# Kernel tuning notes

Hardware: AMD Instinct MI355X
Metric: run time of the kernel (lower is better)

Reference implementation:

```python
import jax, jax.numpy as jnp
import numpy as np

CHEB_K = 2  # Chebyshev polynomial order (init arg cheb_k)


def _avwgcn(x, E, w_pool, b_pool):
    """Adaptive Vertex-Wise Graph Convolution (AGCRN's AVWGCN).
    x: [B, N, C_in], E: [N, D], w_pool: [D, K, C_in, C_out], b_pool: [D, C_out].
    """
    N = E.shape[0]
    # adaptive adjacency from node embeddings
    supports = jax.nn.softmax(jax.nn.relu(E @ E.T), axis=1)  # [N, N]
    support_set = [jnp.eye(N, dtype=x.dtype), supports]
    for _ in range(2, CHEB_K):
        support_set.append(2.0 * supports @ support_set[-1] - support_set[-2])
    supports_k = jnp.stack(support_set)  # [K, N, N]
    # per-node adaptive weights/bias generated from embeddings
    weights = jnp.einsum('nd,dkio->nkio', E, w_pool)  # [N, K, C_in, C_out]
    bias = E @ b_pool  # [N, C_out]
    # graph propagation then per-node adaptive projection
    x_g = jnp.einsum('knm,bmc->bnkc', supports_k, x)  # [B, N, K, C_in]
    return jnp.einsum('bnki,nkio->bno', x_g, weights) + bias  # [B, N, C_out]


def setup_inputs() -> dict:
    key = jax.random.key(0)
    ks = jax.random.split(key, 7)
    B, N, DIN, DOUT, D = 64, 2048, 2, 64, 10
    return {
        'x': jax.random.normal(ks[0], (B, N, DIN), dtype=jnp.float32),
        'state': jax.random.normal(ks[1], (B, N, DOUT), dtype=jnp.float32),
        'node_embeddings': jax.random.normal(ks[2], (N, D), dtype=jnp.float32),
        'gate_w_pool': jax.random.normal(ks[3], (D, CHEB_K, DIN + DOUT, 2 * DOUT), dtype=jnp.float32) * 0.1,
        'gate_b_pool': jax.random.normal(ks[4], (D, 2 * DOUT), dtype=jnp.float32) * 0.1,
        'update_w_pool': jax.random.normal(ks[5], (D, CHEB_K, DIN + DOUT, DOUT), dtype=jnp.float32) * 0.1,
        'update_b_pool': jax.random.normal(ks[6], (D, DOUT), dtype=jnp.float32) * 0.1,
    }


def reference(x, state, node_embeddings, gate_w_pool, gate_b_pool, update_w_pool, update_b_pool):
    hidden_dim = state.shape[-1]
    input_and_state = jnp.concatenate([x, state], axis=-1)  # [B, N, DIN+DOUT]
    z_r = jax.nn.sigmoid(_avwgcn(input_and_state, node_embeddings, gate_w_pool, gate_b_pool))
    z, r = z_r[..., :hidden_dim], z_r[..., hidden_dim:]
    candidate = jnp.concatenate([x, z * state], axis=-1)
    hc = jnp.tanh(_avwgcn(candidate, node_embeddings, update_w_pool, update_b_pool))
    h = r * state + (1.0 - r) * hc
    return h
```

## Files before the change

kernel.cpp:

```cpp
#include <hip/hip_runtime.h>
#include <math.h>

#define N_NODES 2048
#define BATCH   64
#define DIN     2
#define DOUT    64
#define CIN     66
#define CP      68
#define D_EMB   10
#define GOUT    128
#define NCOLS   (BATCH*CP)
#define MK      2048
#define KTOT    132
#define LP      68

typedef __attribute__((ext_vector_type(8))) short bf16x8;
typedef __attribute__((ext_vector_type(8))) unsigned short u16x8;
typedef __attribute__((ext_vector_type(4))) float f32x4;

__device__ __forceinline__ unsigned short f2bf_rn(float f) {
    unsigned u = __builtin_bit_cast(unsigned, f);
    unsigned r = u + 0x7FFFu + ((u >> 16) & 1u);
    return (unsigned short)(r >> 16);
}
__device__ __forceinline__ float bf2f(unsigned short h) {
    unsigned u = ((unsigned)h) << 16;
    return __builtin_bit_cast(float, u);
}

__device__ __forceinline__ void gload_lds16(const void* g, void* l) {
    __builtin_amdgcn_global_load_lds(
        (const __attribute__((address_space(1))) unsigned int*)g,
        (__attribute__((address_space(3))) unsigned int*)l, 16, 0, 0);
}

__global__ __launch_bounds__(256) void supports_kernel(
    const float* __restrict__ E, unsigned short* __restrict__ S_hi)
{
    const int n   = blockIdx.x;
    const int tid = threadIdx.x;

    float en[D_EMB];
#pragma unroll
    for (int d = 0; d < D_EMB; ++d) en[d] = E[n * D_EMB + d];

    float vals[8];
    float mx = -1e30f;
#pragma unroll
    for (int j = 0; j < 8; ++j) {
        const int m = tid + j * 256;
        float dot = 0.f;
#pragma unroll
        for (int d = 0; d < D_EMB; ++d) dot += en[d] * E[m * D_EMB + d];
        dot = fmaxf(dot, 0.f);
        vals[j] = dot;
        mx = fmaxf(mx, dot);
    }

    __shared__ float sred[4];
    for (int off = 32; off > 0; off >>= 1) mx = fmaxf(mx, __shfl_xor(mx, off));
    if ((tid & 63) == 0) sred[tid >> 6] = mx;
    __syncthreads();
    mx = fmaxf(fmaxf(sred[0], sred[1]), fmaxf(sred[2], sred[3]));

    float sum = 0.f;
#pragma unroll
    for (int j = 0; j < 8; ++j) { vals[j] = __expf(vals[j] - mx); sum += vals[j]; }

    __syncthreads();
    for (int off = 32; off > 0; off >>= 1) sum += __shfl_xor(sum, off);
    if ((tid & 63) == 0) sred[tid >> 6] = sum;
    __syncthreads();
    sum = sred[0] + sred[1] + sred[2] + sred[3];

    const float inv = 1.f / sum;
#pragma unroll
    for (int j = 0; j < 8; ++j)
        S_hi[(size_t)n * N_NODES + tid + j * 256] = f2bf_rn(vals[j] * inv);
}

__global__ __launch_bounds__(256) void build_xt_kernel(
    const float* __restrict__ x, const float* __restrict__ state,
    const unsigned short* __restrict__ zs, const int use_zs,
    unsigned short* __restrict__ XT)
{
    const int b   = blockIdx.y;
    const int m0  = blockIdx.x * 64;
    const int tid = threadIdx.x;
    __shared__ float T[64][69];

    {
        const int r = tid >> 2;
        const int q = (tid & 3) * 16;
        if (use_zs) {
            const u16x8 v0 = *(const u16x8*)&zs[((size_t)(m0 + r) * BATCH + b) * DOUT + q];
            const u16x8 v1 = *(const u16x8*)&zs[((size_t)(m0 + r) * BATCH + b) * DOUT + q + 8];
#pragma unroll
            for (int u = 0; u < 8; ++u) {
                T[r][DIN + q + u]     = bf2f(v0[u]);
                T[r][DIN + q + 8 + u] = bf2f(v1[u]);
            }
        } else {
#pragma unroll
            for (int u = 0; u < 4; ++u) {
                const float4 v = *(const float4*)&state[((size_t)b * N_NODES + m0 + r) * DOUT + q + u * 4];
                T[r][DIN + q + u * 4 + 0] = v.x;
                T[r][DIN + q + u * 4 + 1] = v.y;
                T[r][DIN + q + u * 4 + 2] = v.z;
                T[r][DIN + q + u * 4 + 3] = v.w;
            }
        }
    }
    if (tid < 128) {
        const int r = tid >> 1, c = tid & 1;
        T[r][c] = x[((size_t)b * N_NODES + m0 + r) * DIN + c];
        T[r][CIN + c] = 0.f;
    }
    __syncthreads();

    for (int idx = tid; idx < CP * 64; idx += 256) {
        const int c  = idx >> 6;
        const int mm = idx & 63;
        XT[((size_t)(b * CP + c)) * N_NODES + m0 + mm] = f2bf_rn(T[mm][c]);
    }
}

__global__ __launch_bounds__(256) void gemm_mfma_kernel(
    const unsigned short* __restrict__ A,
    const unsigned short* __restrict__ BT, float* __restrict__ C)
{
    __shared__ __align__(16) unsigned short As[4096];
    __shared__ __align__(16) unsigned short Bs[4096];

    const int tid  = threadIdx.x;
    const int lane = tid & 63;
    const int w    = tid >> 6;
    const int wr   = w >> 1, wc = w & 1;
    const int bn   = blockIdx.x;
    const int bm   = blockIdx.y;

    f32x4 acc[4][4];
#pragma unroll
    for (int i = 0; i < 4; ++i)
#pragma unroll
        for (int j = 0; j < 4; ++j) acc[i][j] = (f32x4){0.f, 0.f, 0.f, 0.f};

    const int srow = ((tid >> 6) << 4) + (tid & 15);
    const int scol = ((tid >> 4) & 3) * 8;
    const unsigned a_off0 = (unsigned)(bm * 128 + srow) * MK + scol;
    const unsigned a_off1 = a_off0 + 64u * MK;
    const unsigned b_off0 = (unsigned)(bn * 128 + srow) * MK + scol;
    const unsigned b_off1 = b_off0 + 64u * MK;

    unsigned short* asl0 = As + tid * 8;
    unsigned short* asl1 = As + 2048 + tid * 8;
    unsigned short* bsl0 = Bs + tid * 8;
    unsigned short* bsl1 = Bs + 2048 + tid * 8;

#pragma unroll 1
    for (int k0 = 0; k0 < MK; k0 += 32) {
        gload_lds16(A  + a_off0 + k0, asl0);
        gload_lds16(A  + a_off1 + k0, asl1);
        gload_lds16(BT + b_off0 + k0, bsl0);
        gload_lds16(BT + b_off1 + k0, bsl1);
        __syncthreads();

        bf16x8 af[4], bf[4];
#pragma unroll
        for (int i = 0; i < 4; ++i)
            af[i] = *(const bf16x8*)(As + ((wr * 4 + i) * 64 + lane) * 8);
#pragma unroll
        for (int j = 0; j < 4; ++j)
            bf[j] = *(const bf16x8*)(Bs + ((wc * 4 + j) * 64 + lane) * 8);
#pragma unroll
        for (int i = 0; i < 4; ++i)
#pragma unroll
            for (int j = 0; j < 4; ++j)
                acc[i][j] = __builtin_amdgcn_mfma_f32_16x16x32_bf16(
                    af[i], bf[j], acc[i][j], 0, 0, 0);
        __syncthreads();
    }

    const int crow0 = bm * 128 + wr * 64;
    const int ccol0 = bn * 128 + wc * 64;
#pragma unroll
    for (int i = 0; i < 4; ++i)
#pragma unroll
        for (int j = 0; j < 4; ++j)
#pragma unroll
            for (int r = 0; r < 4; ++r) {
                const int row = crow0 + i * 16 + (lane >> 4) * 4 + r;
                const int col = ccol0 + j * 16 + (lane & 15);
                C[(size_t)row * NCOLS + col] = acc[i][j][r];
            }
}

__global__ __launch_bounds__(256) void gate_transform_kernel(
    const float* __restrict__ E, const float* __restrict__ wp,
    const float* __restrict__ bp, const float* __restrict__ x,
    const float* __restrict__ state, const float* __restrict__ AG,
    unsigned short* __restrict__ ZS, float* __restrict__ Rbuf)
{
    const int n     = blockIdx.x;
    const int ohalf = blockIdx.y;
    const int tid   = threadIdx.x;

    __shared__ float Wl[KTOT * LP];
    __shared__ float Il[KTOT * LP];
    __shared__ float bias_l[64];

    float en[D_EMB];
#pragma unroll
    for (int d = 0; d < D_EMB; ++d) en[d] = E[n * D_EMB + d];

    for (int idx = tid; idx < KTOT * 16; idx += 256) {
        const int kp = idx >> 4;
        const int o4 = (idx & 15) << 2;
        const float* wpp = wp + (size_t)kp * GOUT + ohalf * 64 + o4;
        float s0 = 0.f, s1 = 0.f, s2 = 0.f, s3 = 0.f;
#pragma unroll
        for (int d = 0; d < D_EMB; ++d) {
            const float4 v = *(const float4*)(wpp + (size_t)d * KTOT * GOUT);
            s0 += en[d] * v.x; s1 += en[d] * v.y;
            s2 += en[d] * v.z; s3 += en[d] * v.w;
        }
        *(float4*)&Wl[kp * LP + o4] = make_float4(s0, s1, s2, s3);
    }
    if (tid < 64) {
        float s = 0.f;
#pragma unroll
        for (int d = 0; d < D_EMB; ++d) s += en[d] * bp[d * GOUT + ohalf * 64 + tid];
        bias_l[tid] = s;
    }
    for (int idx = tid; idx < KTOT * BATCH; idx += 256) {
        const int kp = idx % KTOT;
        const int b  = idx / KTOT;
        float v;
        if (kp >= CIN)      v = AG[(size_t)n * NCOLS + b * CP + (kp - CIN)];
        else if (kp >= DIN) v = state[((size_t)b * N_NODES + n) * DOUT + kp - DIN];
        else                v = x[((size_t)b * N_NODES + n) * DIN + kp];
        Il[kp * LP + b] = v;
    }
    __syncthreads();

    const int og = (tid & 15) << 2;
    const int bg = (tid >> 4) << 2;

    float acc[4][4];
#pragma unroll
    for (int i = 0; i < 4; ++i)
#pragma unroll
        for (int j = 0; j < 4; ++j) acc[i][j] = 0.f;

    const float* Wb = Wl + og;
    const float* Ib = Il + bg;
#pragma unroll 4
    for (int kp = 0; kp < KTOT; ++kp) {
        const float4 wv = *(const float4*)(Wb + kp * LP);
        const float4 iv = *(const float4*)(Ib + kp * LP);
        const float wa[4] = {wv.x, wv.y, wv.z, wv.w};
        const float ia[4] = {iv.x, iv.y, iv.z, iv.w};
#pragma unroll
        for (int bi = 0; bi < 4; ++bi)
#pragma unroll
            for (int oi = 0; oi < 4; ++oi) acc[bi][oi] += ia[bi] * wa[oi];
    }

    if (ohalf == 0) {
#pragma unroll
        for (int bi = 0; bi < 4; ++bi) {
            const int b = bg + bi;
            const float4 st4 = *(const float4*)&state[((size_t)b * N_NODES + n) * DOUT + og];
            const float z0 = 1.f / (1.f + __expf(-(acc[bi][0] + bias_l[og + 0])));
            const float z1 = 1.f / (1.f + __expf(-(acc[bi][1] + bias_l[og + 1])));
            const float z2 = 1.f / (1.f + __expf(-(acc[bi][2] + bias_l[og + 2])));
            const float z3 = 1.f / (1.f + __expf(-(acc[bi][3] + bias_l[og + 3])));
            ushort4 zz;
            zz.x = f2bf_rn(z0 * st4.x); zz.y = f2bf_rn(z1 * st4.y);
            zz.z = f2bf_rn(z2 * st4.z); zz.w = f2bf_rn(z3 * st4.w);
            *(ushort4*)&ZS[((size_t)n * BATCH + b) * DOUT + og] = zz;
        }
    } else {
#pragma unroll
        for (int bi = 0; bi < 4; ++bi) {
            const int b = bg + bi;
            float4 rr;
            rr.x = 1.f / (1.f + __expf(-(acc[bi][0] + bias_l[og + 0])));
            rr.y = 1.f / (1.f + __expf(-(acc[bi][1] + bias_l[og + 1])));
            rr.z = 1.f / (1.f + __expf(-(acc[bi][2] + bias_l[og + 2])));
            rr.w = 1.f / (1.f + __expf(-(acc[bi][3] + bias_l[og + 3])));
            *(float4*)&Rbuf[((size_t)n * BATCH + b) * DOUT + og] = rr;
        }
    }
}

__global__ __launch_bounds__(256) void update_final_kernel(
    const float* __restrict__ E, const float* __restrict__ wp,
    const float* __restrict__ bp, const float* __restrict__ x,
    const unsigned short* __restrict__ ZS, const float* __restrict__ AG,
    const float* __restrict__ state, const float* __restrict__ Rbuf,
    float* __restrict__ out)
{
    const int n   = blockIdx.x;
    const int tid = threadIdx.x;

    __shared__ float Wl[KTOT * LP];
    __shared__ float Il[KTOT * LP];
    __shared__ float bias_l[64];

    float en[D_EMB];
#pragma unroll
    for (int d = 0; d < D_EMB; ++d) en[d] = E[n * D_EMB + d];

    for (int idx = tid; idx < KTOT * 16; idx += 256) {
        const int kp = idx >> 4;
        const int o4 = (idx & 15) << 2;
        const float* wpp = wp + (size_t)kp * DOUT + o4;
        float s0 = 0.f, s1 = 0.f, s2 = 0.f, s3 = 0.f;
#pragma unroll
        for (int d = 0; d < D_EMB; ++d) {
            const float4 v = *(const float4*)(wpp + (size_t)d * KTOT * DOUT);
            s0 += en[d] * v.x; s1 += en[d] * v.y;
            s2 += en[d] * v.z; s3 += en[d] * v.w;
        }
        *(float4*)&Wl[kp * LP + o4] = make_float4(s0, s1, s2, s3);
    }
    if (tid < 64) {
        float s = 0.f;
#pragma unroll
        for (int d = 0; d < D_EMB; ++d) s += en[d] * bp[d * DOUT + tid];
        bias_l[tid] = s;
    }
    for (int idx = tid; idx < KTOT * BATCH; idx += 256) {
        const int kp = idx % KTOT;
        const int b  = idx / KTOT;
        float v;
        if (kp >= CIN)      v = AG[(size_t)n * NCOLS + b * CP + (kp - CIN)];
        else if (kp >= DIN) v = bf2f(ZS[((size_t)n * BATCH + b) * DOUT + kp - DIN]);
        else                v = x[((size_t)b * N_NODES + n) * DIN + kp];
        Il[kp * LP + b] = v;
    }
    __syncthreads();

    const int og = (tid & 15) << 2;
    const int bg = (tid >> 4) << 2;

    float acc[4][4];
#pragma unroll
    for (int i = 0; i < 4; ++i)
#pragma unroll
        for (int j = 0; j < 4; ++j) acc[i][j] = 0.f;

    const float* Wb = Wl + og;
    const float* Ib = Il + bg;
#pragma unroll 4
    for (int kp = 0; kp < KTOT; ++kp) {
        const float4 wv = *(const float4*)(Wb + kp * LP);
        const float4 iv = *(const float4*)(Ib + kp * LP);
        const float wa[4] = {wv.x, wv.y, wv.z, wv.w};
        const float ia[4] = {iv.x, iv.y, iv.z, iv.w};
#pragma unroll
        for (int bi = 0; bi < 4; ++bi)
#pragma unroll
            for (int oi = 0; oi < 4; ++oi) acc[bi][oi] += ia[bi] * wa[oi];
    }

#pragma unroll
    for (int bi = 0; bi < 4; ++bi) {
        const int b = bg + bi;
        const float4 r4  = *(const float4*)&Rbuf[((size_t)n * BATCH + b) * DOUT + og];
        const float4 st4 = *(const float4*)&state[((size_t)b * N_NODES + n) * DOUT + og];
        float4 h;
        h.x = r4.x * st4.x + (1.f - r4.x) * tanhf(acc[bi][0] + bias_l[og + 0]);
        h.y = r4.y * st4.y + (1.f - r4.y) * tanhf(acc[bi][1] + bias_l[og + 1]);
        h.z = r4.z * st4.z + (1.f - r4.z) * tanhf(acc[bi][2] + bias_l[og + 2]);
        h.w = r4.w * st4.w + (1.f - r4.w) * tanhf(acc[bi][3] + bias_l[og + 3]);
        *(float4*)&out[((size_t)b * N_NODES + n) * DOUT + og] = h;
    }
}

extern "C" void kernel_launch(void* const* d_in, const int* in_sizes, int n_in,
                              void* d_out, int out_size, void* d_ws, size_t ws_size,
                              hipStream_t stream)
{
    const float* x  = (const float*)d_in[0];
    const float* st = (const float*)d_in[1];
    const float* E  = (const float*)d_in[2];
    const float* gw = (const float*)d_in[3];
    const float* gb = (const float*)d_in[4];
    const float* uw = (const float*)d_in[5];
    const float* ub = (const float*)d_in[6];
    float* out = (float*)d_out;

    unsigned short* S_hi = (unsigned short*)d_ws;
    unsigned short* XT   = S_hi + (size_t)N_NODES * N_NODES;
    float* AG = (float*)(XT + (size_t)NCOLS * N_NODES);
    unsigned short* ZS = (unsigned short*)(AG + (size_t)N_NODES * NCOLS);
    float* Rb = (float*)(ZS + (size_t)N_NODES * BATCH * DOUT);

    supports_kernel<<<N_NODES, 256, 0, stream>>>(E, S_hi);
    build_xt_kernel<<<dim3(N_NODES / 64, BATCH), 256, 0, stream>>>(x, st, ZS, 0, XT);
    gemm_mfma_kernel<<<dim3(NCOLS / 128, N_NODES / 128), 256, 0, stream>>>(S_hi, XT, AG);
    gate_transform_kernel<<<dim3(N_NODES, 2), 256, 0, stream>>>(E, gw, gb, x, st, AG, ZS, Rb);
    build_xt_kernel<<<dim3(N_NODES / 64, BATCH), 256, 0, stream>>>(x, st, ZS, 1, XT);
    gemm_mfma_kernel<<<dim3(NCOLS / 128, N_NODES / 128), 256, 0, stream>>>(S_hi, XT, AG);
    update_final_kernel<<<N_NODES, 256, 0, stream>>>(E, uw, ub, x, ZS, AG, st, Rb, out);
}
```

Before: 572.2 us.

## Move per-node gate/update projections to bf16 MFMA with split-weight precision

Replaces the scalar FP32 per-node projection loops in the gate and update kernels with 16x16x32 bf16 MFMA. Weights are split into hi/lo bf16 parts to keep accuracy, and inputs go into swizzled LDS fragments. A new pre-pass transposes the weight pools so per-node weight generation can use contiguous vector loads. The main GEMM grid is also remapped to a 1D launch with XCD-aware block ordering. The cost is two extra small launches, and the activations are now rounded to bf16, which may add error.

```diff
diff --git a/kernel.cpp b/kernel.cpp
--- a/kernel.cpp
+++ b/kernel.cpp
@@ -12,7 +12,7 @@
 #define NCOLS   (BATCH*CP)
 #define MK      2048
 #define KTOT    132
-#define LP      68
+#define KPAD    136
 
 typedef __attribute__((ext_vector_type(8))) short bf16x8;
 typedef __attribute__((ext_vector_type(8))) unsigned short u16x8;
@@ -32,6 +32,23 @@
     __builtin_amdgcn_global_load_lds(
         (const __attribute__((address_space(1))) unsigned int*)g,
         (__attribute__((address_space(3))) unsigned int*)l, 16, 0, 0);
+}
+
+__device__ __forceinline__ int frag_addr(int strip, int kt, int row, int slice) {
+    const int byte = ((strip * 5 + kt) * 16 + row) * 64 + slice * 16;
+    return byte ^ ((row & 7) << 4);
+}
+
+__global__ __launch_bounds__(256) void transpose_pool_kernel(
+    const float* __restrict__ wp, float* __restrict__ wpT, int OC, int total)
+{
+    const int idx = blockIdx.x * 256 + threadIdx.x;
+    if (idx >= total) return;
+    const int kp   = idx % KPAD;
+    const int rest = idx / KPAD;
+    const int o    = rest % OC;
+    const int d    = rest / OC;
+    wpT[idx] = (kp < KTOT) ? wp[((size_t)d * KTOT + kp) * OC + o] : 0.f;
 }
 
 __global__ __launch_bounds__(256) void supports_kernel(
@@ -136,8 +153,11 @@
     const int lane = tid & 63;
     const int w    = tid >> 6;
     const int wr   = w >> 1, wc = w & 1;
-    const int bn   = blockIdx.x;
-    const int bm   = blockIdx.y;
+
+    const int wg   = blockIdx.x;
+    const int wgid = (wg & 7) * 68 + (wg >> 3);
+    const int bn   = wgid % 34;
+    const int bm   = wgid / 34;
 
     f32x4 acc[4][4];
 #pragma unroll
@@ -195,8 +215,8 @@
             }
 }
 
-__global__ __launch_bounds__(256) void gate_transform_kernel(
-    const float* __restrict__ E, const float* __restrict__ wp,
+__global__ __launch_bounds__(256) void gate_mfma_kernel(
+    const float* __restrict__ E, const float* __restrict__ wpT,
     const float* __restrict__ bp, const float* __restrict__ x,
     const float* __restrict__ state, const float* __restrict__ AG,
     unsigned short* __restrict__ ZS, float* __restrict__ Rbuf)
@@ -205,26 +225,40 @@
     const int ohalf = blockIdx.y;
     const int tid   = threadIdx.x;
 
-    __shared__ float Wl[KTOT * LP];
-    __shared__ float Il[KTOT * LP];
+    __shared__ __align__(16) unsigned short INh[10240];
+    __shared__ __align__(16) unsigned short Whi[10240];
+    __shared__ __align__(16) unsigned short Wlo[10240];
     __shared__ float bias_l[64];
 
     float en[D_EMB];
 #pragma unroll
     for (int d = 0; d < D_EMB; ++d) en[d] = E[n * D_EMB + d];
 
-    for (int idx = tid; idx < KTOT * 16; idx += 256) {
-        const int kp = idx >> 4;
-        const int o4 = (idx & 15) << 2;
-        const float* wpp = wp + (size_t)kp * GOUT + ohalf * 64 + o4;
-        float s0 = 0.f, s1 = 0.f, s2 = 0.f, s3 = 0.f;
-#pragma unroll
-        for (int d = 0; d < D_EMB; ++d) {
-            const float4 v = *(const float4*)(wpp + (size_t)d * KTOT * GOUT);
-            s0 += en[d] * v.x; s1 += en[d] * v.y;
-            s2 += en[d] * v.z; s3 += en[d] * v.w;
-        }
-        *(float4*)&Wl[kp * LP + o4] = make_float4(s0, s1, s2, s3);
+    for (int slot = tid; slot < 1280; slot += 256) {
+        const int o = slot / 20, s = slot % 20;
+        float v[8] = {0.f, 0.f, 0.f, 0.f, 0.f, 0.f, 0.f, 0.f};
+        if (s < 17) {
+            const float* p = wpT + ((size_t)(ohalf * 64 + o)) * KPAD + s * 8;
+#pragma unroll
+            for (int d = 0; d < D_EMB; ++d) {
+                const float4 a = *(const float4*)(p + (size_t)d * GOUT * KPAD);
+                const float4 b = *(const float4*)(p + (size_t)d * GOUT * KPAD + 4);
+                v[0] += en[d] * a.x; v[1] += en[d] * a.y;
+                v[2] += en[d] * a.z; v[3] += en[d] * a.w;
+                v[4] += en[d] * b.x; v[5] += en[d] * b.y;
+                v[6] += en[d] * b.z; v[7] += en[d] * b.w;
+            }
+        }
+        u16x8 hv, lv;
+#pragma unroll
+        for (int u = 0; u < 8; ++u) {
+            const unsigned short h = f2bf_rn(v[u]);
+            hv[u] = h;
+            lv[u] = f2bf_rn(v[u] - bf2f(h));
+        }
+        const int addr = frag_addr(o >> 4, s >> 2, o & 15, s & 3);
+        *(u16x8*)((char*)Whi + addr) = hv;
+        *(u16x8*)((char*)Wlo + addr) = lv;
     }
     if (tid < 64) {
         float s = 0.f;
@@ -232,70 +266,69 @@
         for (int d = 0; d < D_EMB; ++d) s += en[d] * bp[d * GOUT + ohalf * 64 + tid];
         bias_l[tid] = s;
     }
-    for (int idx = tid; idx < KTOT * BATCH; idx += 256) {
-        const int kp = idx % KTOT;
-        const int b  = idx / KTOT;
-        float v;
-        if (kp >= CIN)      v = AG[(size_t)n * NCOLS + b * CP + (kp - CIN)];
-        else if (kp >= DIN) v = state[((size_t)b * N_NODES + n) * DOUT + kp - DIN];
-        else                v = x[((size_t)b * N_NODES + n) * DIN + kp];
-        Il[kp * LP + b] = v;
-    }
-    __syncthreads();
-
-    const int og = (tid & 15) << 2;
-    const int bg = (tid >> 4) << 2;
-
-    float acc[4][4];
-#pragma unroll
-    for (int i = 0; i < 4; ++i)
-#pragma unroll
-        for (int j = 0; j < 4; ++j) acc[i][j] = 0.f;
-
-    const float* Wb = Wl + og;
-    const float* Ib = Il + bg;
-#pragma unroll 4
-    for (int kp = 0; kp < KTOT; ++kp) {
-        const float4 wv = *(const float4*)(Wb + kp * LP);
-        const float4 iv = *(const float4*)(Ib + kp * LP);
-        const float wa[4] = {wv.x, wv.y, wv.z, wv.w};
-        const float ia[4] = {iv.x, iv.y, iv.z, iv.w};
-#pragma unroll
-        for (int bi = 0; bi < 4; ++bi)
-#pragma unroll
-            for (int oi = 0; oi < 4; ++oi) acc[bi][oi] += ia[bi] * wa[oi];
-    }
-
-    if (ohalf == 0) {
-#pragma unroll
-        for (int bi = 0; bi < 4; ++bi) {
-            const int b = bg + bi;
-            const float4 st4 = *(const float4*)&state[((size_t)b * N_NODES + n) * DOUT + og];
-            const float z0 = 1.f / (1.f + __expf(-(acc[bi][0] + bias_l[og + 0])));
-            const float z1 = 1.f / (1.f + __expf(-(acc[bi][1] + bias_l[og + 1])));
-            const float z2 = 1.f / (1.f + __expf(-(acc[bi][2] + bias_l[og + 2])));
-            const float z3 = 1.f / (1.f + __expf(-(acc[bi][3] + bias_l[og + 3])));
-            ushort4 zz;
-            zz.x = f2bf_rn(z0 * st4.x); zz.y = f2bf_rn(z1 * st4.y);
-            zz.z = f2bf_rn(z2 * st4.z); zz.w = f2bf_rn(z3 * st4.w);
-            *(ushort4*)&ZS[((size_t)n * BATCH + b) * DOUT + og] = zz;
-        }
-    } else {
-#pragma unroll
-        for (int bi = 0; bi < 4; ++bi) {
-            const int b = bg + bi;
-            float4 rr;
-            rr.x = 1.f / (1.f + __expf(-(acc[bi][0] + bias_l[og + 0])));
-            rr.y = 1.f / (1.f + __expf(-(acc[bi][1] + bias_l[og + 1])));
-            rr.z = 1.f / (1.f + __expf(-(acc[bi][2] + bias_l[og + 2])));
-            rr.w = 1.f / (1.f + __expf(-(acc[bi][3] + bias_l[og + 3])));
-            *(float4*)&Rbuf[((size_t)n * BATCH + b) * DOUT + og] = rr;
-        }
-    }
-}
-
-__global__ __launch_bounds__(256) void update_final_kernel(
-    const float* __restrict__ E, const float* __restrict__ wp,
+    for (int slot = tid; slot < 1280; slot += 256) {
+        const int b = slot / 20, s = slot % 20;
+        u16x8 hv;
+#pragma unroll
+        for (int u = 0; u < 8; ++u) {
+            const int k = s * 8 + u;
+            float v;
+            if (k < DIN)       v = x[((size_t)b * N_NODES + n) * DIN + k];
+            else if (k < CIN)  v = state[((size_t)b * N_NODES + n) * DOUT + k - DIN];
+            else if (k < KTOT) v = AG[(size_t)n * NCOLS + b * CP + (k - CIN)];
+            else               v = 0.f;
+            hv[u] = f2bf_rn(v);
+        }
+        *(u16x8*)((char*)INh + frag_addr(b >> 4, s >> 2, b & 15, s & 3)) = hv;
+    }
+    __syncthreads();
+
+    const int lane = tid & 63, w = tid >> 6;
+    const int row = lane & 15, sl = lane >> 4;
+
+    bf16x8 af[5];
+#pragma unroll
+    for (int kt = 0; kt < 5; ++kt)
+        af[kt] = *(const bf16x8*)((const char*)INh + frag_addr(w, kt, row, sl));
+
+    f32x4 acc[4];
+#pragma unroll
+    for (int j = 0; j < 4; ++j) acc[j] = (f32x4){0.f, 0.f, 0.f, 0.f};
+
+#pragma unroll
+    for (int j = 0; j < 4; ++j) {
+#pragma unroll
+        for (int kt = 0; kt < 5; ++kt) {
+            const bf16x8 bh = *(const bf16x8*)((const char*)Whi + frag_addr(j, kt, row, sl));
+            acc[j] = __builtin_amdgcn_mfma_f32_16x16x32_bf16(af[kt], bh, acc[j], 0, 0, 0);
+        }
+#pragma unroll
+        for (int kt = 0; kt < 5; ++kt) {
+            const bf16x8 bl = *(const bf16x8*)((const char*)Wlo + frag_addr(j, kt, row, sl));
+            acc[j] = __builtin_amdgcn_mfma_f32_16x16x32_bf16(af[kt], bl, acc[j], 0, 0, 0);
+        }
+    }
+
+#pragma unroll
+    for (int j = 0; j < 4; ++j) {
+        const int ol = j * 16 + row;
+        const float bs = bias_l[ol];
+#pragma unroll
+        for (int r = 0; r < 4; ++r) {
+            const int b = w * 16 + sl * 4 + r;
+            const float sg = 1.f / (1.f + __expf(-(acc[j][r] + bs)));
+            if (ohalf == 0) {
+                ZS[((size_t)n * BATCH + b) * DOUT + ol] =
+                    f2bf_rn(sg * state[((size_t)b * N_NODES + n) * DOUT + ol]);
+            } else {
+                Rbuf[((size_t)n * BATCH + b) * DOUT + ol] = sg;
+            }
+        }
+    }
+}
+
+__global__ __launch_bounds__(256) void update_mfma_kernel(
+    const float* __restrict__ E, const float* __restrict__ wpT,
     const float* __restrict__ bp, const float* __restrict__ x,
     const unsigned short* __restrict__ ZS, const float* __restrict__ AG,
     const float* __restrict__ state, const float* __restrict__ Rbuf,
@@ -304,26 +337,40 @@
     const int n   = blockIdx.x;
     const int tid = threadIdx.x;
 
-    __shared__ float Wl[KTOT * LP];
-    __shared__ float Il[KTOT * LP];
+    __shared__ __align__(16) unsigned short INh[10240];
+    __shared__ __align__(16) unsigned short Whi[10240];
+    __shared__ __align__(16) unsigned short Wlo[10240];
     __shared__ float bias_l[64];
 
     float en[D_EMB];
 #pragma unroll
     for (int d = 0; d < D_EMB; ++d) en[d] = E[n * D_EMB + d];
 
-    for (int idx = tid; idx < KTOT * 16; idx += 256) {
-        const int kp = idx >> 4;
-        const int o4 = (idx & 15) << 2;
-        const float* wpp = wp + (size_t)kp * DOUT + o4;
-        float s0 = 0.f, s1 = 0.f, s2 = 0.f, s3 = 0.f;
-#pragma unroll
-        for (int d = 0; d < D_EMB; ++d) {
-            const float4 v = *(const float4*)(wpp + (size_t)d * KTOT * DOUT);
-            s0 += en[d] * v.x; s1 += en[d] * v.y;
-            s2 += en[d] * v.z; s3 += en[d] * v.w;
-        }
-        *(float4*)&Wl[kp * LP + o4] = make_float4(s0, s1, s2, s3);
+    for (int slot = tid; slot < 1280; slot += 256) {
+        const int o = slot / 20, s = slot % 20;
+        float v[8] = {0.f, 0.f, 0.f, 0.f, 0.f, 0.f, 0.f, 0.f};
+        if (s < 17) {
+            const float* p = wpT + (size_t)o * KPAD + s * 8;
+#pragma unroll
+            for (int d = 0; d < D_EMB; ++d) {
+                const float4 a = *(const float4*)(p + (size_t)d * DOUT * KPAD);
+                const float4 b = *(const float4*)(p + (size_t)d * DOUT * KPAD + 4);
+                v[0] += en[d] * a.x; v[1] += en[d] * a.y;
+                v[2] += en[d] * a.z; v[3] += en[d] * a.w;
+                v[4] += en[d] * b.x; v[5] += en[d] * b.y;
+                v[6] += en[d] * b.z; v[7] += en[d] * b.w;
+            }
+        }
+        u16x8 hv, lv;
+#pragma unroll
+        for (int u = 0; u < 8; ++u) {
+            const unsigned short h = f2bf_rn(v[u]);
+            hv[u] = h;
+            lv[u] = f2bf_rn(v[u] - bf2f(h));
+        }
+        const int addr = frag_addr(o >> 4, s >> 2, o & 15, s & 3);
+        *(u16x8*)((char*)Whi + addr) = hv;
+        *(u16x8*)((char*)Wlo + addr) = lv;
     }
     if (tid < 64) {
         float s = 0.f;
@@ -331,51 +378,61 @@
         for (int d = 0; d < D_EMB; ++d) s += en[d] * bp[d * DOUT + tid];
         bias_l[tid] = s;
     }
-    for (int idx = tid; idx < KTOT * BATCH; idx += 256) {
-        const int kp = idx % KTOT;
-        const int b  = idx / KTOT;
-        float v;
-        if (kp >= CIN)      v = AG[(size_t)n * NCOLS + b * CP + (kp - CIN)];
-        else if (kp >= DIN) v = bf2f(ZS[((size_t)n * BATCH + b) * DOUT + kp - DIN]);
-        else                v = x[((size_t)b * N_NODES + n) * DIN + kp];
-        Il[kp * LP + b] = v;
-    }
-    __syncthreads();
-
-    const int og = (tid & 15) << 2;
-    const int bg = (tid >> 4) << 2;
-
-    float acc[4][4];
-#pragma unroll
-    for (int i = 0; i < 4; ++i)
-#pragma unroll
-        for (int j = 0; j < 4; ++j) acc[i][j] = 0.f;
-
-    const float* Wb = Wl + og;
-    const float* Ib = Il + bg;
-#pragma unroll 4
-    for (int kp = 0; kp < KTOT; ++kp) {
-        const float4 wv = *(const float4*)(Wb + kp * LP);
-        const float4 iv = *(const float4*)(Ib + kp * LP);
-        const float wa[4] = {wv.x, wv.y, wv.z, wv.w};
-        const float ia[4] = {iv.x, iv.y, iv.z, iv.w};
-#pragma unroll
-        for (int bi = 0; bi < 4; ++bi)
-#pragma unroll
-            for (int oi = 0; oi < 4; ++oi) acc[bi][oi] += ia[bi] * wa[oi];
-    }
-
-#pragma unroll
-    for (int bi = 0; bi < 4; ++bi) {
-        const int b = bg + bi;
-        const float4 r4  = *(const float4*)&Rbuf[((size_t)n * BATCH + b) * DOUT + og];
-        const float4 st4 = *(const float4*)&state[((size_t)b * N_NODES + n) * DOUT + og];
-        float4 h;
-        h.x = r4.x * st4.x + (1.f - r4.x) * tanhf(acc[bi][0] + bias_l[og + 0]);
-        h.y = r4.y * st4.y + (1.f - r4.y) * tanhf(acc[bi][1] + bias_l[og + 1]);
-        h.z = r4.z * st4.z + (1.f - r4.z) * tanhf(acc[bi][2] + bias_l[og + 2]);
-        h.w = r4.w * st4.w + (1.f - r4.w) * tanhf(acc[bi][3] + bias_l[og + 3]);
-        *(float4*)&out[((size_t)b * N_NODES + n) * DOUT + og] = h;
+    for (int slot = tid; slot < 1280; slot += 256) {
+        const int b = slot / 20, s = slot % 20;
+        u16x8 hv;
+#pragma unroll
+        for (int u = 0; u < 8; ++u) {
+            const int k = s * 8 + u;
+            float v;
+            if (k < DIN)       v = x[((size_t)b * N_NODES + n) * DIN + k];
+            else if (k < CIN)  v = bf2f(ZS[((size_t)n * BATCH + b) * DOUT + k - DIN]);
+            else if (k < KTOT) v = AG[(size_t)n * NCOLS + b * CP + (k - CIN)];
+            else               v = 0.f;
+            hv[u] = f2bf_rn(v);
+        }
+        *(u16x8*)((char*)INh + frag_addr(b >> 4, s >> 2, b & 15, s & 3)) = hv;
+    }
+    __syncthreads();
+
+    const int lane = tid & 63, w = tid >> 6;
+    const int row = lane & 15, sl = lane >> 4;
+
+    bf16x8 af[5];
+#pragma unroll
+    for (int kt = 0; kt < 5; ++kt)
+        af[kt] = *(const bf16x8*)((const char*)INh + frag_addr(w, kt, row, sl));
+
+    f32x4 acc[4];
+#pragma unroll
+    for (int j = 0; j < 4; ++j) acc[j] = (f32x4){0.f, 0.f, 0.f, 0.f};
+
+#pragma unroll
+    for (int j = 0; j < 4; ++j) {
+#pragma unroll
+        for (int kt = 0; kt < 5; ++kt) {
+            const bf16x8 bh = *(const bf16x8*)((const char*)Whi + frag_addr(j, kt, row, sl));
+            acc[j] = __builtin_amdgcn_mfma_f32_16x16x32_bf16(af[kt], bh, acc[j], 0, 0, 0);
+        }
+#pragma unroll
+        for (int kt = 0; kt < 5; ++kt) {
+            const bf16x8 bl = *(const bf16x8*)((const char*)Wlo + frag_addr(j, kt, row, sl));
+            acc[j] = __builtin_amdgcn_mfma_f32_16x16x32_bf16(af[kt], bl, acc[j], 0, 0, 0);
+        }
+    }
+
+#pragma unroll
+    for (int j = 0; j < 4; ++j) {
+        const int ol = j * 16 + row;
+        const float bs = bias_l[ol];
+#pragma unroll
+        for (int r = 0; r < 4; ++r) {
+            const int b = w * 16 + sl * 4 + r;
+            const float hc = tanhf(acc[j][r] + bs);
+            const float rr = Rbuf[((size_t)n * BATCH + b) * DOUT + ol];
+            const float st = state[((size_t)b * N_NODES + n) * DOUT + ol];
+            out[((size_t)b * N_NODES + n) * DOUT + ol] = rr * st + (1.f - rr) * hc;
+        }
     }
 }
 
@@ -396,13 +453,20 @@
     unsigned short* XT   = S_hi + (size_t)N_NODES * N_NODES;
     float* AG = (float*)(XT + (size_t)NCOLS * N_NODES);
     unsigned short* ZS = (unsigned short*)(AG + (size_t)N_NODES * NCOLS);
-    float* Rb = (float*)(ZS + (size_t)N_NODES * BATCH * DOUT);
+    float* Rb   = (float*)(ZS + (size_t)N_NODES * BATCH * DOUT);
+    float* wpTg = Rb + (size_t)N_NODES * BATCH * DOUT;
+    float* wpTu = wpTg + (size_t)D_EMB * GOUT * KPAD;
+
+    const int tg = D_EMB * GOUT * KPAD;
+    const int tu = D_EMB * DOUT * KPAD;
+    transpose_pool_kernel<<<(tg + 255) / 256, 256, 0, stream>>>(gw, wpTg, GOUT, tg);
+    transpose_pool_kernel<<<(tu + 255) / 256, 256, 0, stream>>>(uw, wpTu, DOUT, tu);
 
     supports_kernel<<<N_NODES, 256, 0, stream>>>(E, S_hi);
     build_xt_kernel<<<dim3(N_NODES / 64, BATCH), 256, 0, stream>>>(x, st, ZS, 0, XT);
-    gemm_mfma_kernel<<<dim3(NCOLS / 128, N_NODES / 128), 256, 0, stream>>>(S_hi, XT, AG);
-    gate_transform_kernel<<<dim3(N_NODES, 2), 256, 0, stream>>>(E, gw, gb, x, st, AG, ZS, Rb);
+    gemm_mfma_kernel<<<544, 256, 0, stream>>>(S_hi, XT, AG);
+    gate_mfma_kernel<<<dim3(N_NODES, 2), 256, 0, stream>>>(E, wpTg, gb, x, st, AG, ZS, Rb);
     build_xt_kernel<<<dim3(N_NODES / 64, BATCH), 256, 0, stream>>>(x, st, ZS, 1, XT);
-    gemm_mfma_kernel<<<dim3(NCOLS / 128, N_NODES / 128), 256, 0, stream>>>(S_hi, XT, AG);
-    update_final_kernel<<<N_NODES, 256, 0, stream>>>(E, uw, ub, x, ZS, AG, st, Rb, out);
-}
+    gemm_mfma_kernel<<<544, 256, 0, stream>>>(S_hi, XT, AG);
+    update_mfma_kernel<<<N_NODES, 256, 0, stream>>>(E, wpTu, ub, x, ZS, AG, st, Rb, out);
+}
```

New measurement: 538.8 us. 5.8% less time.
